# Kernel tuning notes

Hardware: AMD Instinct MI355X
Metric: run time of the kernel (lower is better)

Reference implementation:

```python
import jax, jax.numpy as jnp
import numpy as np

B, AT, NBR = 8, 96, 512
NG, NT = 25, 5            # n_gaussian_triple, n_theta
NANG = NG * NT            # 125, filternet input dim
NF = 128                  # n_filters
NB = 128                  # n_atom_basis


def ssp(x):
    # shifted softplus: ln(0.5*e^x + 0.5) = softplus(x) - ln(2)
    return jax.nn.softplus(x) - jnp.asarray(np.log(2.0), x.dtype)


def setup_inputs() -> dict:
    key = jax.random.key(0)
    ks = jax.random.split(key, 16)
    s = lambda fan_in: 1.0 / np.sqrt(fan_in)
    return {
        "x": jax.random.normal(ks[0], (B, AT, NB), jnp.float32),
        "triple_ijk": jax.random.uniform(ks[1], (B, AT, NBR, NANG), jnp.float32),
        "neighbors_j": jax.random.randint(ks[2], (B, AT, NBR), 0, AT, jnp.int32),
        "neighbors_k": jax.random.randint(ks[3], (B, AT, NBR), 0, AT, jnp.int32),
        "triple_mask": jnp.ones((B, AT, NBR), jnp.float32),
        # filter network (Dense ssp -> Dense linear)
        "W1": jax.random.normal(ks[4], (NANG, NF), jnp.float32) * s(NANG),
        "b1": jnp.zeros((NF,), jnp.float32),
        "W2": jax.random.normal(ks[5], (NF, NF), jnp.float32) * s(NF),
        "b2": jnp.zeros((NF,), jnp.float32),
        # cfconv in2f (no bias) and f2out (ssp activation)
        "Win": jax.random.normal(ks[6], (NB, NF), jnp.float32) * s(NB),
        "Wf2": jax.random.normal(ks[7], (NF, NB), jnp.float32) * s(NF),
        "bf2": jnp.zeros((NB,), jnp.float32),
        # final dense (linear) before residual
        "Wd": jax.random.normal(ks[8], (NB, NB), jnp.float32) * s(NB),
        "bd": jnp.zeros((NB,), jnp.float32),
    }


def _gather_atoms(y, nbh):
    # y: (B, At, F); nbh: (B, At, Nbr) -> (B, At, Nbr, F)
    b, at, nbr = nbh.shape
    idx = nbh.reshape(b, at * nbr, 1)
    return jnp.take_along_axis(y, idx, axis=1).reshape(b, at, nbr, y.shape[-1])


def reference(x, triple_ijk, neighbors_j, neighbors_k, triple_mask,
              W1, b1, W2, b2, Win, Wf2, bf2, Wd, bd):
    # filter network on angular/radial triple features -> (B, At, Nbr, NF)
    W_triple = ssp(triple_ijk @ W1 + b1) @ W2 + b2
    # in2f
    y = x @ Win                                  # (B, At, NF)
    y_j = _gather_atoms(y, neighbors_j)          # (B, At, Nbr, NF)
    y_k = _gather_atoms(y, neighbors_k)          # (B, At, Nbr, NF)
    # element-wise continuous-filter conv over triples, mask padded triples
    yt = y_j * y_k * W_triple * triple_mask[..., None]
    agg = jnp.sum(yt, axis=2)                    # sum-aggregate over triples
    v = ssp(agg @ Wf2 + bf2)                     # f2out with shifted softplus
    v = v @ Wd + bd                              # interaction dense
    return x + v                                 # residual
```

## Files before the change

kernel.cpp:

```cpp
#include <hip/hip_runtime.h>
#include <math.h>

#define B_    8
#define AT_   96
#define NBR_  512
#define NANG_ 125
#define NF_   128
#define NB_   128
#define TN    32
#define NCHUNK 4
#define CROWS (NBR_ / NCHUNK)
#define TSTRIDE 136
#define JSTRIDE 132

typedef __attribute__((ext_vector_type(8))) short bf16x8;
typedef __attribute__((ext_vector_type(4))) float f32x4;

__device__ __forceinline__ short f2bf(float f) {
    union { float f; unsigned u; } x; x.f = f;
    return (short)((x.u + 0x8000u) >> 16);
}

__device__ __forceinline__ float sspf(float x) {
    float p = __builtin_amdgcn_exp2f(x * 1.44269504088896340736f);
    float l = __builtin_amdgcn_logf(1.0f + p);
    return 0.69314718055994530942f * l - 0.69314718055994530942f;
}

__global__ __launch_bounds__(128) void prep_kernel(
    const float* __restrict__ x, const float* __restrict__ Win,
    const float* __restrict__ W1, const float* __restrict__ W2,
    float* __restrict__ y, short* __restrict__ w1p, short* __restrict__ w2p)
{
    __shared__ float xs[4][NB_];
    int blk = blockIdx.x, tid = threadIdx.x;
    if (blk < 192) {
        int row0 = blk * 4;
        #pragma unroll
        for (int r = 0; r < 4; r++) xs[r][tid] = x[(row0 + r) * NB_ + tid];
        __syncthreads();
        float a0 = 0.f, a1 = 0.f, a2 = 0.f, a3 = 0.f;
        #pragma unroll 8
        for (int k = 0; k < NB_; k++) {
            float w = Win[k * NF_ + tid];
            a0 = fmaf(xs[0][k], w, a0);
            a1 = fmaf(xs[1][k], w, a1);
            a2 = fmaf(xs[2][k], w, a2);
            a3 = fmaf(xs[3][k], w, a3);
        }
        y[(row0 + 0) * NF_ + tid] = a0;
        y[(row0 + 1) * NF_ + tid] = a1;
        y[(row0 + 2) * NF_ + tid] = a2;
        y[(row0 + 3) * NF_ + tid] = a3;
    } else {
        int t = (blk - 192) * 128 + tid;
        int j = t & 7, lane = (t >> 3) & 63, ks = (t >> 9) & 3, ct = t >> 11;
        int k = ks * 32 + (lane >> 4) * 8 + j;
        int n = ct * 16 + (lane & 15);
        w1p[t] = (k < NANG_) ? f2bf(W1[k * NF_ + n]) : (short)0;
        w2p[t] = f2bf(W2[k * NF_ + n]);
    }
}

__global__ __launch_bounds__(256) void triple_partial(
    const float* __restrict__ trip,
    const int* __restrict__ nbj, const int* __restrict__ nbk,
    const float* __restrict__ maskg,
    const float* __restrict__ b1g, const float* __restrict__ b2g,
    const float* __restrict__ y, const short* __restrict__ w1p,
    const short* __restrict__ w2p, float* __restrict__ pagg)
{
    __shared__ short ts[TN * TSTRIDE];
    __shared__ short hs[TN * TSTRIDE];
    __shared__ float yjk[TN * JSTRIDE];

    const int tid = threadIdx.x;
    const int wave = tid >> 6, lane = tid & 63;
    const int quad = lane >> 4, col = lane & 15;
    const int blk = blockIdx.x;
    const int bid = blk >> 2, c = blk & 3;
    const int b = bid / AT_;

    const float* tpc = trip + (long)bid * NBR_ * NANG_ + (long)c * CROWS * NANG_;
    const int nb_base = bid * NBR_ + c * CROWS;

    const int ct0 = 2 * wave, ct1 = 2 * wave + 1;
    const int f0 = ct0 * 16 + col, f1 = ct1 * 16 + col;
    const float bias1_0 = b1g[f0], bias1_1 = b1g[f1];
    const float bias2_0 = b2g[f0], bias2_1 = b2g[f1];

    const int yrow = tid >> 3, ypart = tid & 7;

    if (tid < 96) {
        int r = tid / 3, kp = 125 + (tid - 3 * r);
        ts[r * TSTRIDE + kp] = 0;
    }

    float accw0 = 0.f, accw1 = 0.f;

    for (int nt = 0; nt < CROWS / TN; nt++) {
        const float* tp = tpc + nt * TN * NANG_;
        const int nrow0 = nb_base + nt * TN;

        f32x4 t0 = ((const f32x4*)tp)[tid];
        f32x4 t1 = ((const f32x4*)tp)[tid + 256];
        f32x4 t2 = ((const f32x4*)tp)[tid + 512];
        f32x4 t3 = {0.f, 0.f, 0.f, 0.f};
        if (tid < 232) t3 = ((const f32x4*)tp)[tid + 768];

        const int jj = nbj[nrow0 + yrow], kk = nbk[nrow0 + yrow];
        const float m = maskg[nrow0 + yrow];
        const float* yjp = y + (b * AT_ + jj) * NF_ + ypart * 16;
        const float* ykp = y + (b * AT_ + kk) * NF_ + ypart * 16;
        f32x4 j0 = ((const f32x4*)yjp)[0], j1 = ((const f32x4*)yjp)[1];
        f32x4 j2 = ((const f32x4*)yjp)[2], j3 = ((const f32x4*)yjp)[3];
        f32x4 k0 = ((const f32x4*)ykp)[0], k1 = ((const f32x4*)ykp)[1];
        f32x4 k2 = ((const f32x4*)ykp)[2], k3 = ((const f32x4*)ykp)[3];

        __syncthreads();

        {
            int f = tid * 4, r = f / 125, k = f - r * 125;
            ts[r * TSTRIDE + k] = f2bf(t0.x); if (++k == 125) { k = 0; ++r; }
            ts[r * TSTRIDE + k] = f2bf(t0.y); if (++k == 125) { k = 0; ++r; }
            ts[r * TSTRIDE + k] = f2bf(t0.z); if (++k == 125) { k = 0; ++r; }
            ts[r * TSTRIDE + k] = f2bf(t0.w);
        }
        {
            int f = (tid + 256) * 4, r = f / 125, k = f - r * 125;
            ts[r * TSTRIDE + k] = f2bf(t1.x); if (++k == 125) { k = 0; ++r; }
            ts[r * TSTRIDE + k] = f2bf(t1.y); if (++k == 125) { k = 0; ++r; }
            ts[r * TSTRIDE + k] = f2bf(t1.z); if (++k == 125) { k = 0; ++r; }
            ts[r * TSTRIDE + k] = f2bf(t1.w);
        }
        {
            int f = (tid + 512) * 4, r = f / 125, k = f - r * 125;
            ts[r * TSTRIDE + k] = f2bf(t2.x); if (++k == 125) { k = 0; ++r; }
            ts[r * TSTRIDE + k] = f2bf(t2.y); if (++k == 125) { k = 0; ++r; }
            ts[r * TSTRIDE + k] = f2bf(t2.z); if (++k == 125) { k = 0; ++r; }
            ts[r * TSTRIDE + k] = f2bf(t2.w);
        }
        if (tid < 232) {
            int f = (tid + 768) * 4, r = f / 125, k = f - r * 125;
            ts[r * TSTRIDE + k] = f2bf(t3.x); if (++k == 125) { k = 0; ++r; }
            ts[r * TSTRIDE + k] = f2bf(t3.y); if (++k == 125) { k = 0; ++r; }
            ts[r * TSTRIDE + k] = f2bf(t3.z); if (++k == 125) { k = 0; ++r; }
            ts[r * TSTRIDE + k] = f2bf(t3.w);
        }
        {
            float* d = &yjk[yrow * JSTRIDE + ypart * 16];
            *(f32x4*)(d + 0)  = j0 * k0 * m;
            *(f32x4*)(d + 4)  = j1 * k1 * m;
            *(f32x4*)(d + 8)  = j2 * k2 * m;
            *(f32x4*)(d + 12) = j3 * k3 * m;
        }
        __syncthreads();

        f32x4 d00 = {0,0,0,0}, d01 = {0,0,0,0}, d10 = {0,0,0,0}, d11 = {0,0,0,0};
        #pragma unroll
        for (int ks = 0; ks < 4; ks++) {
            bf16x8 a0 = *(const bf16x8*)&ts[(     col) * TSTRIDE + ks * 32 + quad * 8];
            bf16x8 a1 = *(const bf16x8*)&ts[(16 + col) * TSTRIDE + ks * 32 + quad * 8];
            bf16x8 w0 = *(const bf16x8*)&w1p[(ct0 * 4 + ks) * 512 + lane * 8];
            bf16x8 w1 = *(const bf16x8*)&w1p[(ct1 * 4 + ks) * 512 + lane * 8];
            d00 = __builtin_amdgcn_mfma_f32_16x16x32_bf16(a0, w0, d00, 0, 0, 0);
            d01 = __builtin_amdgcn_mfma_f32_16x16x32_bf16(a0, w1, d01, 0, 0, 0);
            d10 = __builtin_amdgcn_mfma_f32_16x16x32_bf16(a1, w0, d10, 0, 0, 0);
            d11 = __builtin_amdgcn_mfma_f32_16x16x32_bf16(a1, w1, d11, 0, 0, 0);
        }
        #pragma unroll
        for (int r = 0; r < 4; r++) {
            int row0 = quad * 4 + r, row1 = 16 + quad * 4 + r;
            hs[row0 * TSTRIDE + f0] = f2bf(sspf(d00[r] + bias1_0));
            hs[row0 * TSTRIDE + f1] = f2bf(sspf(d01[r] + bias1_1));
            hs[row1 * TSTRIDE + f0] = f2bf(sspf(d10[r] + bias1_0));
            hs[row1 * TSTRIDE + f1] = f2bf(sspf(d11[r] + bias1_1));
        }
        __syncthreads();

        f32x4 e00 = {0,0,0,0}, e01 = {0,0,0,0}, e10 = {0,0,0,0}, e11 = {0,0,0,0};
        #pragma unroll
        for (int ks = 0; ks < 4; ks++) {
            bf16x8 a0 = *(const bf16x8*)&hs[(     col) * TSTRIDE + ks * 32 + quad * 8];
            bf16x8 a1 = *(const bf16x8*)&hs[(16 + col) * TSTRIDE + ks * 32 + quad * 8];
            bf16x8 w0 = *(const bf16x8*)&w2p[(ct0 * 4 + ks) * 512 + lane * 8];
            bf16x8 w1 = *(const bf16x8*)&w2p[(ct1 * 4 + ks) * 512 + lane * 8];
            e00 = __builtin_amdgcn_mfma_f32_16x16x32_bf16(a0, w0, e00, 0, 0, 0);
            e01 = __builtin_amdgcn_mfma_f32_16x16x32_bf16(a0, w1, e01, 0, 0, 0);
            e10 = __builtin_amdgcn_mfma_f32_16x16x32_bf16(a1, w0, e10, 0, 0, 0);
            e11 = __builtin_amdgcn_mfma_f32_16x16x32_bf16(a1, w1, e11, 0, 0, 0);
        }
        #pragma unroll
        for (int r = 0; r < 4; r++) {
            int row0 = quad * 4 + r, row1 = 16 + quad * 4 + r;
            accw0 += (e00[r] + bias2_0) * yjk[row0 * JSTRIDE + f0];
            accw1 += (e01[r] + bias2_1) * yjk[row0 * JSTRIDE + f1];
            accw0 += (e10[r] + bias2_0) * yjk[row1 * JSTRIDE + f0];
            accw1 += (e11[r] + bias2_1) * yjk[row1 * JSTRIDE + f1];
        }
    }

    accw0 += __shfl_xor(accw0, 16, 64);
    accw0 += __shfl_xor(accw0, 32, 64);
    accw1 += __shfl_xor(accw1, 16, 64);
    accw1 += __shfl_xor(accw1, 32, 64);
    if (quad == 0) {
        pagg[blk * NF_ + f0] = accw0;
        pagg[blk * NF_ + f1] = accw1;
    }
}

__global__ __launch_bounds__(128) void finish_kernel(
    const float* __restrict__ x, const float* __restrict__ pagg,
    const float* __restrict__ Wf2, const float* __restrict__ bf2,
    const float* __restrict__ Wd, const float* __restrict__ bd,
    float* __restrict__ out)
{
    __shared__ float aggs[NF_];
    __shared__ float t1s[NF_];
    int bid = blockIdx.x, f = threadIdx.x;
    float a = pagg[(bid * 4 + 0) * NF_ + f] + pagg[(bid * 4 + 1) * NF_ + f]
            + pagg[(bid * 4 + 2) * NF_ + f] + pagg[(bid * 4 + 3) * NF_ + f];
    aggs[f] = a;
    __syncthreads();
    float acc = 0.f;
    #pragma unroll 8
    for (int k = 0; k < NF_; k++) acc = fmaf(aggs[k], Wf2[k * NB_ + f], acc);
    t1s[f] = sspf(acc + bf2[f]);
    __syncthreads();
    acc = 0.f;
    #pragma unroll 8
    for (int k = 0; k < NB_; k++) acc = fmaf(t1s[k], Wd[k * NB_ + f], acc);
    out[bid * NB_ + f] = x[bid * NB_ + f] + acc + bd[f];
}

extern "C" void kernel_launch(void* const* d_in, const int* in_sizes, int n_in,
                              void* d_out, int out_size, void* d_ws, size_t ws_size,
                              hipStream_t stream) {
    const float* x    = (const float*)d_in[0];
    const float* trip = (const float*)d_in[1];
    const int*   nbj  = (const int*)d_in[2];
    const int*   nbk  = (const int*)d_in[3];
    const float* mask = (const float*)d_in[4];
    const float* W1   = (const float*)d_in[5];
    const float* b1   = (const float*)d_in[6];
    const float* W2   = (const float*)d_in[7];
    const float* b2   = (const float*)d_in[8];
    const float* Win  = (const float*)d_in[9];
    const float* Wf2  = (const float*)d_in[10];
    const float* bf2  = (const float*)d_in[11];
    const float* Wd   = (const float*)d_in[12];
    const float* bd   = (const float*)d_in[13];
    float* out = (float*)d_out;

    char* ws = (char*)d_ws;
    float* y    = (float*)ws;
    short* w1p  = (short*)(ws + 393216);
    short* w2p  = (short*)(ws + 393216 + 32768);
    float* pagg = (float*)(ws + 393216 + 65536);

    prep_kernel<<<320, 128, 0, stream>>>(x, Win, W1, W2, y, w1p, w2p);
    triple_partial<<<B_ * AT_ * NCHUNK, 256, 0, stream>>>(trip, nbj, nbk, mask,
        b1, b2, y, w1p, w2p, pagg);
    finish_kernel<<<B_ * AT_, 128, 0, stream>>>(x, pagg, Wf2, bf2, Wd, bd, out);
}
```

Baseline: 345.8 us.

## Load triple features directly into MFMA fragments and double-buffer shared tiles

The triple-feature tile is no longer staged through shared memory. Each lane loads its A-fragment straight from global memory with unaligned 16-byte loads, converts it with packed bf16 conversion instructions, and prefetches the next k-slice and next tile while the MFMAs run. The W1/W2 fragments are hoisted into registers once per block, the neighbour indices are prefetched one tile ahead, and the hs/yjk buffers are double-buffered so one barrier per tile is dropped. The grid now uses 2 chunks instead of 4, halving the partial sums, with a launch-bounds occupancy hint added. The costs are more register pressure, uncoalesced global loads of the 125-wide rows, and a special case so the last lane of the last block does not read past the end of the input.

```diff
diff --git a/kernel.cpp b/kernel.cpp
--- a/kernel.cpp
+++ b/kernel.cpp
@@ -8,8 +8,9 @@
 #define NF_   128
 #define NB_   128
 #define TN    32
-#define NCHUNK 4
+#define NCHUNK 2
 #define CROWS (NBR_ / NCHUNK)
+#define NTI   (CROWS / TN)
 #define TSTRIDE 136
 #define JSTRIDE 132
 
@@ -25,6 +26,21 @@
     float p = __builtin_amdgcn_exp2f(x * 1.44269504088896340736f);
     float l = __builtin_amdgcn_logf(1.0f + p);
     return 0.69314718055994530942f * l - 0.69314718055994530942f;
+}
+
+__device__ __forceinline__ f32x4 ld4u(const float* p) {
+    f32x4 v; __builtin_memcpy(&v, p, 16); return v;
+}
+
+__device__ __forceinline__ bf16x8 cvt8(f32x4 lo, f32x4 hi) {
+    unsigned r0, r1, r2, r3;
+    asm("v_cvt_pk_bf16_f32 %0, %1, %2" : "=v"(r0) : "v"(lo.x), "v"(lo.y));
+    asm("v_cvt_pk_bf16_f32 %0, %1, %2" : "=v"(r1) : "v"(lo.z), "v"(lo.w));
+    asm("v_cvt_pk_bf16_f32 %0, %1, %2" : "=v"(r2) : "v"(hi.x), "v"(hi.y));
+    asm("v_cvt_pk_bf16_f32 %0, %1, %2" : "=v"(r3) : "v"(hi.z), "v"(hi.w));
+    typedef __attribute__((ext_vector_type(4))) unsigned u32x4;
+    u32x4 r = { r0, r1, r2, r3 };
+    return __builtin_bit_cast(bf16x8, r);
 }
 
 __global__ __launch_bounds__(128) void prep_kernel(
@@ -62,7 +78,7 @@
     }
 }
 
-__global__ __launch_bounds__(256) void triple_partial(
+__global__ __launch_bounds__(256, 2) void triple_partial(
     const float* __restrict__ trip,
     const int* __restrict__ nbj, const int* __restrict__ nbk,
     const float* __restrict__ maskg,
@@ -70,15 +86,14 @@
     const float* __restrict__ y, const short* __restrict__ w1p,
     const short* __restrict__ w2p, float* __restrict__ pagg)
 {
-    __shared__ short ts[TN * TSTRIDE];
-    __shared__ short hs[TN * TSTRIDE];
-    __shared__ float yjk[TN * JSTRIDE];
+    __shared__ short hs[2][TN * TSTRIDE];
+    __shared__ float yjk[2][TN * JSTRIDE];
 
     const int tid = threadIdx.x;
     const int wave = tid >> 6, lane = tid & 63;
     const int quad = lane >> 4, col = lane & 15;
     const int blk = blockIdx.x;
-    const int bid = blk >> 2, c = blk & 3;
+    const int bid = blk >> 1, c = blk & 1;
     const int b = bid / AT_;
 
     const float* tpc = trip + (long)bid * NBR_ * NANG_ + (long)c * CROWS * NANG_;
@@ -90,114 +105,105 @@
     const float bias2_0 = b2g[f0], bias2_1 = b2g[f1];
 
     const int yrow = tid >> 3, ypart = tid & 7;
-
-    if (tid < 96) {
-        int r = tid / 3, kp = 125 + (tid - 3 * r);
-        ts[r * TSTRIDE + kp] = 0;
-    }
+    const bool lastblk = (blk == B_ * AT_ * NCHUNK - 1);
+
+    bf16x8 w1f0[4], w1f1[4], w2f0[4], w2f1[4];
+    #pragma unroll
+    for (int ks = 0; ks < 4; ks++) {
+        w1f0[ks] = *(const bf16x8*)&w1p[(ct0 * 4 + ks) * 512 + lane * 8];
+        w1f1[ks] = *(const bf16x8*)&w1p[(ct1 * 4 + ks) * 512 + lane * 8];
+        w2f0[ks] = *(const bf16x8*)&w2p[(ct0 * 4 + ks) * 512 + lane * 8];
+        w2f1[ks] = *(const bf16x8*)&w2p[(ct1 * 4 + ks) * 512 + lane * 8];
+    }
+
+    int jj = nbj[nb_base + yrow];
+    int kk = nbk[nb_base + yrow];
+    float mk = maskg[nb_base + yrow];
+
+    const float* arow = tpc + col * NANG_;
+    f32x4 pa0 = ld4u(arow + quad * 8);
+    f32x4 pa1 = ld4u(arow + quad * 8 + 4);
+    f32x4 pb0 = ld4u(arow + 16 * NANG_ + quad * 8);
+    f32x4 pb1 = ld4u(arow + 16 * NANG_ + quad * 8 + 4);
 
     float accw0 = 0.f, accw1 = 0.f;
-
-    for (int nt = 0; nt < CROWS / TN; nt++) {
-        const float* tp = tpc + nt * TN * NANG_;
-        const int nrow0 = nb_base + nt * TN;
-
-        f32x4 t0 = ((const f32x4*)tp)[tid];
-        f32x4 t1 = ((const f32x4*)tp)[tid + 256];
-        f32x4 t2 = ((const f32x4*)tp)[tid + 512];
-        f32x4 t3 = {0.f, 0.f, 0.f, 0.f};
-        if (tid < 232) t3 = ((const f32x4*)tp)[tid + 768];
-
-        const int jj = nbj[nrow0 + yrow], kk = nbk[nrow0 + yrow];
-        const float m = maskg[nrow0 + yrow];
+    int cur = 0;
+
+    for (int nt = 0; nt < NTI; nt++) {
         const float* yjp = y + (b * AT_ + jj) * NF_ + ypart * 16;
         const float* ykp = y + (b * AT_ + kk) * NF_ + ypart * 16;
         f32x4 j0 = ((const f32x4*)yjp)[0], j1 = ((const f32x4*)yjp)[1];
         f32x4 j2 = ((const f32x4*)yjp)[2], j3 = ((const f32x4*)yjp)[3];
         f32x4 k0 = ((const f32x4*)ykp)[0], k1 = ((const f32x4*)ykp)[1];
         f32x4 k2 = ((const f32x4*)ykp)[2], k3 = ((const f32x4*)ykp)[3];
-
-        __syncthreads();
+        const float mc = mk;
+        if (nt + 1 < NTI) {
+            jj = nbj[nb_base + (nt + 1) * TN + yrow];
+            kk = nbk[nb_base + (nt + 1) * TN + yrow];
+            mk = maskg[nb_base + (nt + 1) * TN + yrow];
+        }
+
+        const bool lt = lastblk && (nt == NTI - 1);
+        const float* anext = (nt == NTI - 1) ? arow : (arow + TN * NANG_);
+
+        f32x4 d00 = {0,0,0,0}, d01 = {0,0,0,0}, d10 = {0,0,0,0}, d11 = {0,0,0,0};
+        #pragma unroll
+        for (int ks = 0; ks < 4; ks++) {
+            bf16x8 a0 = cvt8(pa0, pa1);
+            bf16x8 a1 = cvt8(pb0, pb1);
+            const float* pn = (ks < 3) ? arow : anext;
+            const int    ko = (ks < 3) ? ((ks + 1) * 32 + quad * 8) : (quad * 8);
+            pa0 = ld4u(pn + ko);
+            pa1 = ld4u(pn + ko + 4);
+            pb0 = ld4u(pn + 16 * NANG_ + ko);
+            if (ks == 2 && lt && lane == 63) {
+                pb1 = (f32x4){ pn[16 * NANG_ + ko + 4], 0.f, 0.f, 0.f };
+            } else {
+                pb1 = ld4u(pn + 16 * NANG_ + ko + 4);
+            }
+            d00 = __builtin_amdgcn_mfma_f32_16x16x32_bf16(a0, w1f0[ks], d00, 0, 0, 0);
+            d01 = __builtin_amdgcn_mfma_f32_16x16x32_bf16(a0, w1f1[ks], d01, 0, 0, 0);
+            d10 = __builtin_amdgcn_mfma_f32_16x16x32_bf16(a1, w1f0[ks], d10, 0, 0, 0);
+            d11 = __builtin_amdgcn_mfma_f32_16x16x32_bf16(a1, w1f1[ks], d11, 0, 0, 0);
+        }
+        arow = anext;
 
         {
-            int f = tid * 4, r = f / 125, k = f - r * 125;
-            ts[r * TSTRIDE + k] = f2bf(t0.x); if (++k == 125) { k = 0; ++r; }
-            ts[r * TSTRIDE + k] = f2bf(t0.y); if (++k == 125) { k = 0; ++r; }
-            ts[r * TSTRIDE + k] = f2bf(t0.z); if (++k == 125) { k = 0; ++r; }
-            ts[r * TSTRIDE + k] = f2bf(t0.w);
-        }
-        {
-            int f = (tid + 256) * 4, r = f / 125, k = f - r * 125;
-            ts[r * TSTRIDE + k] = f2bf(t1.x); if (++k == 125) { k = 0; ++r; }
-            ts[r * TSTRIDE + k] = f2bf(t1.y); if (++k == 125) { k = 0; ++r; }
-            ts[r * TSTRIDE + k] = f2bf(t1.z); if (++k == 125) { k = 0; ++r; }
-            ts[r * TSTRIDE + k] = f2bf(t1.w);
-        }
-        {
-            int f = (tid + 512) * 4, r = f / 125, k = f - r * 125;
-            ts[r * TSTRIDE + k] = f2bf(t2.x); if (++k == 125) { k = 0; ++r; }
-            ts[r * TSTRIDE + k] = f2bf(t2.y); if (++k == 125) { k = 0; ++r; }
-            ts[r * TSTRIDE + k] = f2bf(t2.z); if (++k == 125) { k = 0; ++r; }
-            ts[r * TSTRIDE + k] = f2bf(t2.w);
-        }
-        if (tid < 232) {
-            int f = (tid + 768) * 4, r = f / 125, k = f - r * 125;
-            ts[r * TSTRIDE + k] = f2bf(t3.x); if (++k == 125) { k = 0; ++r; }
-            ts[r * TSTRIDE + k] = f2bf(t3.y); if (++k == 125) { k = 0; ++r; }
-            ts[r * TSTRIDE + k] = f2bf(t3.z); if (++k == 125) { k = 0; ++r; }
-            ts[r * TSTRIDE + k] = f2bf(t3.w);
-        }
-        {
-            float* d = &yjk[yrow * JSTRIDE + ypart * 16];
-            *(f32x4*)(d + 0)  = j0 * k0 * m;
-            *(f32x4*)(d + 4)  = j1 * k1 * m;
-            *(f32x4*)(d + 8)  = j2 * k2 * m;
-            *(f32x4*)(d + 12) = j3 * k3 * m;
-        }
-        __syncthreads();
-
-        f32x4 d00 = {0,0,0,0}, d01 = {0,0,0,0}, d10 = {0,0,0,0}, d11 = {0,0,0,0};
-        #pragma unroll
-        for (int ks = 0; ks < 4; ks++) {
-            bf16x8 a0 = *(const bf16x8*)&ts[(     col) * TSTRIDE + ks * 32 + quad * 8];
-            bf16x8 a1 = *(const bf16x8*)&ts[(16 + col) * TSTRIDE + ks * 32 + quad * 8];
-            bf16x8 w0 = *(const bf16x8*)&w1p[(ct0 * 4 + ks) * 512 + lane * 8];
-            bf16x8 w1 = *(const bf16x8*)&w1p[(ct1 * 4 + ks) * 512 + lane * 8];
-            d00 = __builtin_amdgcn_mfma_f32_16x16x32_bf16(a0, w0, d00, 0, 0, 0);
-            d01 = __builtin_amdgcn_mfma_f32_16x16x32_bf16(a0, w1, d01, 0, 0, 0);
-            d10 = __builtin_amdgcn_mfma_f32_16x16x32_bf16(a1, w0, d10, 0, 0, 0);
-            d11 = __builtin_amdgcn_mfma_f32_16x16x32_bf16(a1, w1, d11, 0, 0, 0);
+            float* d = &yjk[cur][yrow * JSTRIDE + ypart * 16];
+            *(f32x4*)(d + 0)  = j0 * k0 * mc;
+            *(f32x4*)(d + 4)  = j1 * k1 * mc;
+            *(f32x4*)(d + 8)  = j2 * k2 * mc;
+            *(f32x4*)(d + 12) = j3 * k3 * mc;
         }
         #pragma unroll
         for (int r = 0; r < 4; r++) {
             int row0 = quad * 4 + r, row1 = 16 + quad * 4 + r;
-            hs[row0 * TSTRIDE + f0] = f2bf(sspf(d00[r] + bias1_0));
-            hs[row0 * TSTRIDE + f1] = f2bf(sspf(d01[r] + bias1_1));
-            hs[row1 * TSTRIDE + f0] = f2bf(sspf(d10[r] + bias1_0));
-            hs[row1 * TSTRIDE + f1] = f2bf(sspf(d11[r] + bias1_1));
+            hs[cur][row0 * TSTRIDE + f0] = f2bf(sspf(d00[r] + bias1_0));
+            hs[cur][row0 * TSTRIDE + f1] = f2bf(sspf(d01[r] + bias1_1));
+            hs[cur][row1 * TSTRIDE + f0] = f2bf(sspf(d10[r] + bias1_0));
+            hs[cur][row1 * TSTRIDE + f1] = f2bf(sspf(d11[r] + bias1_1));
         }
         __syncthreads();
 
         f32x4 e00 = {0,0,0,0}, e01 = {0,0,0,0}, e10 = {0,0,0,0}, e11 = {0,0,0,0};
         #pragma unroll
         for (int ks = 0; ks < 4; ks++) {
-            bf16x8 a0 = *(const bf16x8*)&hs[(     col) * TSTRIDE + ks * 32 + quad * 8];
-            bf16x8 a1 = *(const bf16x8*)&hs[(16 + col) * TSTRIDE + ks * 32 + quad * 8];
-            bf16x8 w0 = *(const bf16x8*)&w2p[(ct0 * 4 + ks) * 512 + lane * 8];
-            bf16x8 w1 = *(const bf16x8*)&w2p[(ct1 * 4 + ks) * 512 + lane * 8];
-            e00 = __builtin_amdgcn_mfma_f32_16x16x32_bf16(a0, w0, e00, 0, 0, 0);
-            e01 = __builtin_amdgcn_mfma_f32_16x16x32_bf16(a0, w1, e01, 0, 0, 0);
-            e10 = __builtin_amdgcn_mfma_f32_16x16x32_bf16(a1, w0, e10, 0, 0, 0);
-            e11 = __builtin_amdgcn_mfma_f32_16x16x32_bf16(a1, w1, e11, 0, 0, 0);
+            bf16x8 a0 = *(const bf16x8*)&hs[cur][(     col) * TSTRIDE + ks * 32 + quad * 8];
+            bf16x8 a1 = *(const bf16x8*)&hs[cur][(16 + col) * TSTRIDE + ks * 32 + quad * 8];
+            e00 = __builtin_amdgcn_mfma_f32_16x16x32_bf16(a0, w2f0[ks], e00, 0, 0, 0);
+            e01 = __builtin_amdgcn_mfma_f32_16x16x32_bf16(a0, w2f1[ks], e01, 0, 0, 0);
+            e10 = __builtin_amdgcn_mfma_f32_16x16x32_bf16(a1, w2f0[ks], e10, 0, 0, 0);
+            e11 = __builtin_amdgcn_mfma_f32_16x16x32_bf16(a1, w2f1[ks], e11, 0, 0, 0);
         }
         #pragma unroll
         for (int r = 0; r < 4; r++) {
             int row0 = quad * 4 + r, row1 = 16 + quad * 4 + r;
-            accw0 += (e00[r] + bias2_0) * yjk[row0 * JSTRIDE + f0];
-            accw1 += (e01[r] + bias2_1) * yjk[row0 * JSTRIDE + f1];
-            accw0 += (e10[r] + bias2_0) * yjk[row1 * JSTRIDE + f0];
-            accw1 += (e11[r] + bias2_1) * yjk[row1 * JSTRIDE + f1];
-        }
+            accw0 += (e00[r] + bias2_0) * yjk[cur][row0 * JSTRIDE + f0];
+            accw1 += (e01[r] + bias2_1) * yjk[cur][row0 * JSTRIDE + f1];
+            accw0 += (e10[r] + bias2_0) * yjk[cur][row1 * JSTRIDE + f0];
+            accw1 += (e11[r] + bias2_1) * yjk[cur][row1 * JSTRIDE + f1];
+        }
+        cur ^= 1;
     }
 
     accw0 += __shfl_xor(accw0, 16, 64);
@@ -219,8 +225,7 @@
     __shared__ float aggs[NF_];
     __shared__ float t1s[NF_];
     int bid = blockIdx.x, f = threadIdx.x;
-    float a = pagg[(bid * 4 + 0) * NF_ + f] + pagg[(bid * 4 + 1) * NF_ + f]
-            + pagg[(bid * 4 + 2) * NF_ + f] + pagg[(bid * 4 + 3) * NF_ + f];
+    float a = pagg[(bid * 2 + 0) * NF_ + f] + pagg[(bid * 2 + 1) * NF_ + f];
     aggs[f] = a;
     __syncthreads();
     float acc = 0.f;
```

Measured after the change: 397.3 us. 14.9% more time.
